# Optimization experiments

Measured on AMD Instinct MI355X. Metric: run time of the kernel, lower is better.

## Reference

```python
import jax, jax.numpy as jnp
import numpy as np

COMMITMENT_COST = 0.25
EPS = 1e-10


def setup_inputs() -> dict:
    key = jax.random.key(0)
    k1, k2 = jax.random.split(key)
    B, C, H, W = 16, 64, 128, 128          # C == embedding_dim
    K, D = 512, 64                          # codebook size, embedding_dim
    inputs = jax.random.normal(k1, (B, C, H, W), dtype=jnp.float32)
    # nn.Embedding init: uniform(-1/K, 1/K)
    embedding = jax.random.uniform(k2, (K, D), dtype=jnp.float32,
                                   minval=-1.0 / K, maxval=1.0 / K)
    return {"inputs": inputs, "embedding": embedding}


def reference(inputs, embedding):
    # NCHW -> NHWC, flatten to tokens [N, D]
    x = jnp.transpose(inputs, (0, 2, 3, 1))
    nhwc_shape = x.shape
    flat = x.reshape(-1, embedding.shape[1])                       # [N, D]

    distances = (jnp.sum(flat * flat, axis=1, keepdims=True)
                 + jnp.sum(embedding * embedding, axis=1)
                 - 2.0 * flat @ embedding.T)
    idx = jnp.argmin(distances, axis=1)                            # [N]

    # one-hot encodings (returned), quantized via direct gather
    encodings = jax.nn.one_hot(idx, embedding.shape[0], dtype=flat.dtype)  # [N, K]
    quantized = embedding[idx].reshape(nhwc_shape)                 # [B,H,W,D]

    e_latent = jnp.mean((jax.lax.stop_gradient(quantized) - x) ** 2)
    q_latent = jnp.mean((quantized - jax.lax.stop_gradient(x)) ** 2)
    loss = q_latent + COMMITMENT_COST * e_latent

    # straight-through estimator
    quantized_st = x + jax.lax.stop_gradient(quantized - x)

    avg_probs = jnp.mean(encodings, axis=0)                        # [K]
    perplexity = jnp.exp(-jnp.sum(avg_probs * jnp.log(avg_probs + EPS)))

    return (loss, jnp.transpose(quantized_st, (0, 3, 1, 2)), perplexity, encodings)
```

## Files before the change

kernel.cpp:

```cpp
#include <hip/hip_runtime.h>
#include <math.h>


#define NTOK    262144
#define KCODES  512
#define DDIM    64
#define CSTRIDE 16384
#define IMG     1048576
#define QOFF    1
#define POFF    16777217
#define EOFF    16777218
#define EWS     5120
#define SUBFLT  32768

__device__ __forceinline__ float np_pairwise_sq64(const float* v) {
    float r[8];
#pragma unroll
    for (int j = 0; j < 8; ++j) r[j] = __fmul_rn(v[j], v[j]);
#pragma unroll
    for (int i = 8; i < 64; i += 8) {
#pragma unroll
        for (int j = 0; j < 8; ++j)
            r[j] = __fadd_rn(r[j], __fmul_rn(v[i + j], v[i + j]));
    }
    float s01 = __fadd_rn(r[0], r[1]);
    float s23 = __fadd_rn(r[2], r[3]);
    float s45 = __fadd_rn(r[4], r[5]);
    float s67 = __fadd_rn(r[6], r[7]);
    return __fadd_rn(__fadd_rn(s01, s23), __fadd_rn(s45, s67));
}

__global__ __launch_bounds__(256) void vq_prep(const float* __restrict__ emb,
                                               float* __restrict__ ws) {
    const int tid = threadIdx.x, blk = blockIdx.x;
    if (blk < 8) {
#pragma unroll
        for (int ii = 0; ii < 16; ++ii) {
            int t = blk * 4096 + ii * 256 + tid;
            ws[EWS + t] = emb[(size_t)(t & 511) * DDIM + (t >> 9)];
        }
    } else {
#pragma unroll
        for (int r = 0; r < 2; ++r) {
            const int k = tid * 2 + r;
            const float* e = emb + (size_t)k * DDIM;
            float v[64];
#pragma unroll
            for (int i = 0; i < 64; ++i) v[i] = e[i];
            ws[512 + k] = np_pairwise_sq64(v);
        }
    }
}

__global__ __launch_bounds__(256, 3) void vq_main(const float* __restrict__ in,
                                                  const float* __restrict__ emb,
                                                  float* __restrict__ out,
                                                  float* __restrict__ ws) {
    __shared__ float4 xs4[1024];
    __shared__ float4 es4[2048];
    __shared__ float  ash[64];
    __shared__ int    idx_sh[64];
    __shared__ float  red[4];

    const float* xsf = (const float*)xs4;
    const int tid = threadIdx.x, blk = blockIdx.x;
    const int i = tid >> 5, j = tid & 31;
    const int T0 = blk * 64, b = T0 >> 14, hw0 = T0 & 16383;

    {
        const float4* gx = (const float4*)(in + (size_t)b * IMG + hw0);
#pragma unroll
        for (int jj = 0; jj < 4; ++jj) {
            int t = tid + jj * 256;
            int c = t >> 4, q = t & 15;
            xs4[t] = gx[(size_t)c * (CSTRIDE / 4) + q];
        }
    }
    __syncthreads();

    if (tid < 64) {
        float v[64];
#pragma unroll
        for (int c = 0; c < 64; ++c) v[c] = xsf[c * 64 + tid];
        ash[tid] = np_pairwise_sq64(v);
    }
    __syncthreads();

    float av[8];
    float dmin[8]; int idx[8];
#pragma unroll
    for (int tt = 0; tt < 8; ++tt) {
        av[tt] = ash[8 * i + tt];
        dmin[tt] = 3.402823466e38f; idx[tt] = 0;
    }

    float4* sub4 = (float4*)(out + EOFF + (size_t)blk * SUBFLT);
    const float4 z4 = make_float4(0.f, 0.f, 0.f, 0.f);

#pragma unroll 1
    for (int ch = 0; ch < 4; ++ch) {
        __syncthreads();
        {
            const float4* ge = (const float4*)(ws + EWS + ch * 128);
#pragma unroll
            for (int jj = 0; jj < 8; ++jj) {
                int t = tid + jj * 256;
                int d = t >> 5, q = t & 31;
                es4[t] = ge[(size_t)d * 128 + q];
            }
        }
        __syncthreads();

#pragma unroll
        for (int ii = 0; ii < 8; ++ii)
            sub4[ch * 2048 + ii * 256 + tid] = z4;

        float acc[8][4];
#pragma unroll
        for (int tt = 0; tt < 8; ++tt)
#pragma unroll
            for (int cc = 0; cc < 4; ++cc) acc[tt][cc] = 0.f;

        const float4* xr = xs4 + 2 * i;
        const float4* er = es4 + j;
#pragma unroll 4
        for (int d = 0; d < 64; ++d) {
            float4 xa = xr[d * 16], xb = xr[d * 16 + 1];
            float4 ea = er[d * 32];
            float xv[8] = {xa.x,xa.y,xa.z,xa.w,xb.x,xb.y,xb.z,xb.w};
            float ev[4] = {ea.x,ea.y,ea.z,ea.w};
#pragma unroll
            for (int tt = 0; tt < 8; ++tt)
#pragma unroll
                for (int cc = 0; cc < 4; ++cc)
                    acc[tt][cc] = fmaf(xv[tt], ev[cc], acc[tt][cc]);
        }

        float bk[4];
        {
            float4 u0 = *(const float4*)(ws + 512 + ch * 128 + 4 * j);
            bk[0]=u0.x; bk[1]=u0.y; bk[2]=u0.z; bk[3]=u0.w;
        }
        const int cbase = ch * 128 + 4 * j;
#pragma unroll
        for (int cc = 0; cc < 4; ++cc) {
#pragma unroll
            for (int tt = 0; tt < 8; ++tt) {
                float t2 = __fadd_rn(av[tt], bk[cc]);
                float dd = fmaf(-2.0f, acc[tt][cc], t2);
                if (dd < dmin[tt]) { dmin[tt] = dd; idx[tt] = cbase + cc; }
            }
        }
    }

#pragma unroll
    for (int m = 1; m < 32; m <<= 1) {
#pragma unroll
        for (int tt = 0; tt < 8; ++tt) {
            float od = __shfl_xor(dmin[tt], m, 64);
            int   oi = __shfl_xor(idx[tt],  m, 64);
            if (od < dmin[tt] || (od == dmin[tt] && oi < idx[tt])) {
                dmin[tt] = od; idx[tt] = oi;
            }
        }
    }
    if (j == 0) {
#pragma unroll
        for (int tt = 0; tt < 8; ++tt) idx_sh[8 * i + tt] = idx[tt];
    }
    __syncthreads();

    const int tl = tid & 63, chh = (tid >> 6) * 16;
    const int id = idx_sh[tl];
    if (tid < 64) atomicAdd((int*)ws + id, 1);

    float*       q  = out + QOFF + (size_t)b * IMG + hw0 + tl;
    const float* e0 = emb + (size_t)id * DDIM + chh;

    float lsum = 0.f;
#pragma unroll
    for (int cc = 0; cc < 16; ++cc) {
        float x   = xsf[(chh + cc) * 64 + tl];
        float dqx = __fsub_rn(e0[cc], x);
        lsum = __fadd_rn(lsum, __fmul_rn(dqx, dqx));
        q[(size_t)(chh + cc) * CSTRIDE] = __fadd_rn(x, dqx);
    }
#pragma unroll
    for (int off = 32; off > 0; off >>= 1) lsum += __shfl_down(lsum, off, 64);
    if ((tid & 63) == 0) red[tid >> 6] = lsum;
    __syncthreads();
    if (tid == 0) ws[1024 + blk] = red[0] + red[1] + red[2] + red[3];

    if (tid < 64) {
        const int ix = idx_sh[tid];
        float4 v = make_float4(0.f, 0.f, 0.f, 0.f);
        ((float*)&v)[ix & 3] = 1.0f;
        sub4[tid * 128 + (ix >> 2)] = v;
    }
}

__global__ void vq_final(float* __restrict__ out, const float* __restrict__ ws) {
    __shared__ float sl[512], sp[512];
    int t = threadIdx.x;
    float s = 0.f;
#pragma unroll
    for (int r = 0; r < 8; ++r) s += ws[1024 + t + 512 * r];
    sl[t] = s;
    int cnt = ((const int*)ws)[t];
    float p = (float)cnt * (1.0f / 262144.0f);
    sp[t] = p * logf(p + 1e-10f);
    __syncthreads();
    for (int off = 256; off > 0; off >>= 1) {
        if (t < off) { sl[t] += sl[t + off]; sp[t] += sp[t + off]; }
        __syncthreads();
    }
    if (t == 0) {
        float m = sl[0] * (1.0f / 16777216.0f);
        out[0]    = __fadd_rn(m, __fmul_rn(0.25f, m));
        out[POFF] = expf(-sp[0]);
    }
}

extern "C" void kernel_launch(void* const* d_in, const int* in_sizes, int n_in,
                              void* d_out, int out_size, void* d_ws, size_t ws_size,
                              hipStream_t stream) {
    const float* in  = (const float*)d_in[0];
    const float* emb = (const float*)d_in[1];
    float* out = (float*)d_out;
    float* ws  = (float*)d_ws;

    hipMemsetAsync(d_ws, 0, 512 * sizeof(int), stream);
    hipLaunchKernelGGL(vq_prep,  dim3(9),    dim3(256), 0, stream, emb, ws);
    hipLaunchKernelGGL(vq_main,  dim3(4096), dim3(256), 0, stream, in, emb, out, ws);
    hipLaunchKernelGGL(vq_final, dim3(1),    dim3(512), 0, stream, out, ws);
}
```

Measured before the change: 805.9 us.

## Compute codebook distances with bf16 MFMA and write one-hot in single pass

```diff
diff --git a/kernel.cpp b/kernel.cpp
--- a/kernel.cpp
+++ b/kernel.cpp
@@ -10,8 +10,16 @@
 #define QOFF    1
 #define POFF    16777217
 #define EOFF    16777218
-#define EWS     5120
+#define EBF     8192
 #define SUBFLT  32768
+
+typedef short bf16x8 __attribute__((ext_vector_type(8)));
+typedef float f32x4  __attribute__((ext_vector_type(4)));
+
+__device__ __forceinline__ unsigned short f2bf(float f) {
+    unsigned u = __float_as_uint(f);
+    return (unsigned short)((u + 0x7fffu + ((u >> 16) & 1u)) >> 16);
+}
 
 __device__ __forceinline__ float np_pairwise_sq64(const float* v) {
     float r[8];
@@ -34,10 +42,11 @@
                                                float* __restrict__ ws) {
     const int tid = threadIdx.x, blk = blockIdx.x;
     if (blk < 8) {
+        unsigned short* ebf = (unsigned short*)(ws + EBF);
 #pragma unroll
         for (int ii = 0; ii < 16; ++ii) {
             int t = blk * 4096 + ii * 256 + tid;
-            ws[EWS + t] = emb[(size_t)(t & 511) * DDIM + (t >> 9)];
+            ebf[t] = f2bf(emb[t]);
         }
     } else {
 #pragma unroll
@@ -52,23 +61,22 @@
     }
 }
 
-__global__ __launch_bounds__(256, 3) void vq_main(const float* __restrict__ in,
-                                                  const float* __restrict__ emb,
-                                                  float* __restrict__ out,
-                                                  float* __restrict__ ws) {
-    __shared__ float4 xs4[1024];
-    __shared__ float4 es4[2048];
-    __shared__ float  ash[64];
-    __shared__ int    idx_sh[64];
-    __shared__ float  red[4];
-
-    const float* xsf = (const float*)xs4;
+__global__ __launch_bounds__(256) void vq_main(const float* __restrict__ in,
+                                               const float* __restrict__ emb,
+                                               float* __restrict__ out,
+                                               float* __restrict__ ws) {
+    __shared__ float          xs[64 * 64];
+    __shared__ unsigned short xbf[64 * 68];
+    __shared__ float          bsh[512];
+    __shared__ int            idx_sh[64];
+    __shared__ float          red[4];
+
     const int tid = threadIdx.x, blk = blockIdx.x;
-    const int i = tid >> 5, j = tid & 31;
     const int T0 = blk * 64, b = T0 >> 14, hw0 = T0 & 16383;
 
     {
         const float4* gx = (const float4*)(in + (size_t)b * IMG + hw0);
+        float4* xs4 = (float4*)xs;
 #pragma unroll
         for (int jj = 0; jj < 4; ++jj) {
             int t = tid + jj * 256;
@@ -76,97 +84,61 @@
             xs4[t] = gx[(size_t)c * (CSTRIDE / 4) + q];
         }
     }
-    __syncthreads();
-
-    if (tid < 64) {
-        float v[64];
-#pragma unroll
-        for (int c = 0; c < 64; ++c) v[c] = xsf[c * 64 + tid];
-        ash[tid] = np_pairwise_sq64(v);
-    }
-    __syncthreads();
-
-    float av[8];
-    float dmin[8]; int idx[8];
-#pragma unroll
-    for (int tt = 0; tt < 8; ++tt) {
-        av[tt] = ash[8 * i + tt];
-        dmin[tt] = 3.402823466e38f; idx[tt] = 0;
-    }
-
-    float4* sub4 = (float4*)(out + EOFF + (size_t)blk * SUBFLT);
-    const float4 z4 = make_float4(0.f, 0.f, 0.f, 0.f);
-
-#pragma unroll 1
-    for (int ch = 0; ch < 4; ++ch) {
-        __syncthreads();
-        {
-            const float4* ge = (const float4*)(ws + EWS + ch * 128);
-#pragma unroll
-            for (int jj = 0; jj < 8; ++jj) {
-                int t = tid + jj * 256;
-                int d = t >> 5, q = t & 31;
-                es4[t] = ge[(size_t)d * 128 + q];
+    bsh[tid]       = ws[512 + tid];
+    bsh[256 + tid] = ws[768 + tid];
+    __syncthreads();
+
+    {
+        const int t = tid & 63, d0 = (tid >> 6) * 16;
+#pragma unroll
+        for (int dd = 0; dd < 16; ++dd)
+            xbf[t * 68 + d0 + dd] = f2bf(xs[(d0 + dd) * 64 + t]);
+    }
+    __syncthreads();
+
+    const int l = tid & 63, w = tid >> 6;
+    const int lm = l & 15, lg = l >> 4;
+
+    const bf16x8 a0 = *(const bf16x8*)(xbf + (w * 16 + lm) * 68 + lg * 8);
+    const bf16x8 a1 = *(const bf16x8*)(xbf + (w * 16 + lm) * 68 + 32 + lg * 8);
+
+    const unsigned short* ebf = (const unsigned short*)(ws + EBF);
+    const unsigned short* ep  = ebf + lm * 64 + lg * 8;
+
+    float dmin[4]; int idx[4];
+#pragma unroll
+    for (int r = 0; r < 4; ++r) { dmin[r] = 3.402823466e38f; idx[r] = 0; }
+    const f32x4 zero = {0.f, 0.f, 0.f, 0.f};
+
+#pragma unroll 4
+    for (int nt = 0; nt < 32; ++nt) {
+        bf16x8 b0 = *(const bf16x8*)(ep + nt * 1024);
+        bf16x8 b1 = *(const bf16x8*)(ep + nt * 1024 + 32);
+        f32x4 acc = __builtin_amdgcn_mfma_f32_16x16x32_bf16(a0, b0, zero, 0, 0, 0);
+        acc       = __builtin_amdgcn_mfma_f32_16x16x32_bf16(a1, b1, acc,  0, 0, 0);
+        const int   code = nt * 16 + lm;
+        const float bk   = bsh[code];
+#pragma unroll
+        for (int r = 0; r < 4; ++r) {
+            float s = fmaf(-2.0f, acc[r], bk);
+            if (s < dmin[r]) { dmin[r] = s; idx[r] = code; }
+        }
+    }
+
+#pragma unroll
+    for (int m = 1; m < 16; m <<= 1) {
+#pragma unroll
+        for (int r = 0; r < 4; ++r) {
+            float od = __shfl_xor(dmin[r], m, 64);
+            int   oi = __shfl_xor(idx[r],  m, 64);
+            if (od < dmin[r] || (od == dmin[r] && oi < idx[r])) {
+                dmin[r] = od; idx[r] = oi;
             }
         }
-        __syncthreads();
-
-#pragma unroll
-        for (int ii = 0; ii < 8; ++ii)
-            sub4[ch * 2048 + ii * 256 + tid] = z4;
-
-        float acc[8][4];
-#pragma unroll
-        for (int tt = 0; tt < 8; ++tt)
-#pragma unroll
-            for (int cc = 0; cc < 4; ++cc) acc[tt][cc] = 0.f;
-
-        const float4* xr = xs4 + 2 * i;
-        const float4* er = es4 + j;
-#pragma unroll 4
-        for (int d = 0; d < 64; ++d) {
-            float4 xa = xr[d * 16], xb = xr[d * 16 + 1];
-            float4 ea = er[d * 32];
-            float xv[8] = {xa.x,xa.y,xa.z,xa.w,xb.x,xb.y,xb.z,xb.w};
-            float ev[4] = {ea.x,ea.y,ea.z,ea.w};
-#pragma unroll
-            for (int tt = 0; tt < 8; ++tt)
-#pragma unroll
-                for (int cc = 0; cc < 4; ++cc)
-                    acc[tt][cc] = fmaf(xv[tt], ev[cc], acc[tt][cc]);
-        }
-
-        float bk[4];
-        {
-            float4 u0 = *(const float4*)(ws + 512 + ch * 128 + 4 * j);
-            bk[0]=u0.x; bk[1]=u0.y; bk[2]=u0.z; bk[3]=u0.w;
-        }
-        const int cbase = ch * 128 + 4 * j;
-#pragma unroll
-        for (int cc = 0; cc < 4; ++cc) {
-#pragma unroll
-            for (int tt = 0; tt < 8; ++tt) {
-                float t2 = __fadd_rn(av[tt], bk[cc]);
-                float dd = fmaf(-2.0f, acc[tt][cc], t2);
-                if (dd < dmin[tt]) { dmin[tt] = dd; idx[tt] = cbase + cc; }
-            }
-        }
-    }
-
-#pragma unroll
-    for (int m = 1; m < 32; m <<= 1) {
-#pragma unroll
-        for (int tt = 0; tt < 8; ++tt) {
-            float od = __shfl_xor(dmin[tt], m, 64);
-            int   oi = __shfl_xor(idx[tt],  m, 64);
-            if (od < dmin[tt] || (od == dmin[tt] && oi < idx[tt])) {
-                dmin[tt] = od; idx[tt] = oi;
-            }
-        }
-    }
-    if (j == 0) {
-#pragma unroll
-        for (int tt = 0; tt < 8; ++tt) idx_sh[8 * i + tt] = idx[tt];
+    }
+    if (lm == 0) {
+#pragma unroll
+        for (int r = 0; r < 4; ++r) idx_sh[w * 16 + lg * 4 + r] = idx[r];
     }
     __syncthreads();
 
@@ -180,7 +152,7 @@
     float lsum = 0.f;
 #pragma unroll
     for (int cc = 0; cc < 16; ++cc) {
-        float x   = xsf[(chh + cc) * 64 + tl];
+        float x   = xs[(chh + cc) * 64 + tl];
         float dqx = __fsub_rn(e0[cc], x);
         lsum = __fadd_rn(lsum, __fmul_rn(dqx, dqx));
         q[(size_t)(chh + cc) * CSTRIDE] = __fadd_rn(x, dqx);
@@ -191,11 +163,18 @@
     __syncthreads();
     if (tid == 0) ws[1024 + blk] = red[0] + red[1] + red[2] + red[3];
 
-    if (tid < 64) {
-        const int ix = idx_sh[tid];
-        float4 v = make_float4(0.f, 0.f, 0.f, 0.f);
-        ((float*)&v)[ix & 3] = 1.0f;
-        sub4[tid * 128 + (ix >> 2)] = v;
+    float4* s4 = (float4*)(out + EOFF + (size_t)blk * SUBFLT);
+#pragma unroll 4
+    for (int ii = 0; ii < 32; ++ii) {
+        int jj = ii * 256 + tid;
+        int ix = idx_sh[jj >> 7];
+        int c0 = (jj & 127) << 2;
+        float4 v;
+        v.x = (c0     == ix) ? 1.0f : 0.0f;
+        v.y = (c0 + 1 == ix) ? 1.0f : 0.0f;
+        v.z = (c0 + 2 == ix) ? 1.0f : 0.0f;
+        v.w = (c0 + 3 == ix) ? 1.0f : 0.0f;
+        s4[jj] = v;
     }
 }
 
```

New measurement: 754.1 us. -6.4%, faster.
